# Optimization experiments

Hardware: AMD Instinct MI355X
Metric: run time of the kernel (lower is better)

## Reference

```python
import jax, jax.numpy as jnp
import numpy as np

KS = 2            # kernel_size
NUM_SHARED = 3    # len(num_shared_channels)
NBR_PARAM = 3     # nbr_param_layers
COUT = 128        # num_shared_channels[-1] == num_inputs
NUM_INPUTS = 128
D_R = 320         # ts2vec_output_dims
GEN_LEN = NBR_PARAM * COUT * COUT * KS


def _causal_conv(x, w, b, d):
    # x: [N, Ci, T], w: [Co, Ci, K], b: [Co]; left-pad (K-1)*d == pad+chomp in torch
    N, Ci, T = x.shape
    K = w.shape[-1]
    pad = (K - 1) * d
    xp = jnp.pad(x, ((0, 0), (0, 0), (pad, 0)))
    out = jnp.zeros((N, w.shape[0], T), dtype=x.dtype)
    for k in range(K):  # K==2, tiny static loop
        out = out + jnp.einsum('oc,nct->not', w[:, :, k], xp[:, :, k * d:k * d + T])
    return out + b[None, :, None]


def _causal_conv_group(x, w, d):
    # groups=N conv with per-sample weights. x: [N, C, T], w: [N, Co, C, K], no bias
    N, C, T = x.shape
    K = w.shape[-1]
    pad = (K - 1) * d
    xp = jnp.pad(x, ((0, 0), (0, 0), (pad, 0)))
    out = jnp.zeros((N, w.shape[1], T), dtype=x.dtype)
    for k in range(K):
        out = out + jnp.einsum('noc,nct->not', w[..., k], xp[:, :, k * d:k * d + T])
    return out


def setup_inputs() -> dict:
    key = jax.random.key(0)
    ks = jax.random.split(key, 12)
    N, T = 16, 1024
    x = jax.random.normal(ks[0], (N, T, NUM_INPUTS), dtype=jnp.float32)
    r = jax.random.normal(ks[1], (N, D_R), dtype=jnp.float32)
    # shared TemporalBlock params (in==out==COUT, so no downsample conv)
    wscale = 1.0 / np.sqrt(COUT * KS)
    shared_w1 = wscale * jax.random.normal(ks[2], (NUM_SHARED, COUT, COUT, KS), dtype=jnp.float32)
    shared_b1 = 0.01 * jax.random.normal(ks[3], (NUM_SHARED, COUT), dtype=jnp.float32)
    shared_w2 = wscale * jax.random.normal(ks[4], (NUM_SHARED, COUT, COUT, KS), dtype=jnp.float32)
    shared_b2 = 0.01 * jax.random.normal(ks[5], (NUM_SHARED, COUT), dtype=jnp.float32)
    # hypernetwork (f_param_generator) + additive base weights (last_conv_layers)
    fparam_W = 0.01 * jax.random.normal(ks[6], (GEN_LEN, D_R), dtype=jnp.float32)
    fparam_b = 0.01 * jax.random.normal(ks[7], (GEN_LEN,), dtype=jnp.float32)
    last_bias = 0.001 * jax.random.normal(ks[8], (GEN_LEN,), dtype=jnp.float32) + 1.0 / (KS * COUT)
    # output head
    lin_W = (1.0 / np.sqrt(COUT)) * jax.random.normal(ks[9], (NUM_INPUTS, COUT), dtype=jnp.float32)
    lin_b = 0.01 * jax.random.normal(ks[10], (NUM_INPUTS,), dtype=jnp.float32)
    return {"x": x, "r": r, "f_out_same_in_size": 1,
            "shared_w1": shared_w1, "shared_b1": shared_b1,
            "shared_w2": shared_w2, "shared_b2": shared_b2,
            "fparam_W": fparam_W, "fparam_b": fparam_b, "last_bias": last_bias,
            "lin_W": lin_W, "lin_b": lin_b}


def reference(x, r, f_out_same_in_size, shared_w1, shared_b1, shared_w2, shared_b2,
              fparam_W, fparam_b, last_bias, lin_W, lin_b):
    N, T, _ = x.shape
    h = jnp.swapaxes(x, 1, 2)  # [N, C, T]
    # shared TemporalBlocks (dropout p=0 -> identity)
    for i in range(NUM_SHARED):
        d = 2 ** i
        res = h
        a = jax.nn.relu(_causal_conv(h, shared_w1[i], shared_b1[i], d))
        a = jax.nn.relu(_causal_conv(a, shared_w2[i], shared_b2[i], d))
        h = jax.nn.relu(a + res)
    # hypernet-generated per-sample grouped conv layers
    gen = r @ fparam_W.T + fparam_b + last_bias           # [N, GEN_LEN]
    allw = gen.reshape(NBR_PARAM, N, COUT, COUT, KS)      # same layout as torch .view
    for i in range(NBR_PARAM):
        d = 2 ** (NUM_SHARED + i)
        res = h
        c = _causal_conv_group(h, allw[i], d)
        h = jax.nn.relu(jax.nn.relu(c) + res)             # relu(dropout(relu(c)) + res), p=0
    out = jnp.einsum('nct,oc->nto', h, lin_W) + lin_b     # [N, T, NUM_INPUTS]
    if not f_out_same_in_size:
        out = out[:, -1, :]
    return out
```

## Files before the change

kernel.cpp:

```cpp
#include <hip/hip_runtime.h>

#define NB    16
#define TLEN  1024
#define CCH   128
#define DR    320

typedef _Float16 h8 __attribute__((ext_vector_type(8)));
typedef _Float16 h4 __attribute__((ext_vector_type(4)));
typedef _Float16 h2 __attribute__((ext_vector_type(2)));
typedef float    f4 __attribute__((ext_vector_type(4)));

__device__ __forceinline__ void gload16h(const _Float16* g, _Float16* l) {
  __builtin_amdgcn_global_load_lds(
      (const __attribute__((address_space(1))) void*)g,
      (__attribute__((address_space(3))) void*)l, 16, 0, 0);
}
__device__ __forceinline__ void gload16f(const float* g, float* l) {
  __builtin_amdgcn_global_load_lds(
      (const __attribute__((address_space(1))) void*)g,
      (__attribute__((address_space(3))) void*)l, 16, 0, 0);
}

__global__ __launch_bounds__(256) void k_init(const float* __restrict__ x,
                                              const float* __restrict__ w1,
                                              const float* __restrict__ w2,
                                              const float* __restrict__ linw,
                                              const float* __restrict__ fb,
                                              const float* __restrict__ lb,
                                              _Float16* __restrict__ h0,
                                              _Float16* __restrict__ Wsh,
                                              _Float16* __restrict__ linWh,
                                              float* __restrict__ fblb2) {
  int i = blockIdx.x * 256 + threadIdx.x;
  const float4* src = (const float4*)x + (size_t)i * 2;
  float4 a = src[0], b = src[1];
  h8 v;
  v[0] = (_Float16)a.x; v[1] = (_Float16)a.y; v[2] = (_Float16)a.z; v[3] = (_Float16)a.w;
  v[4] = (_Float16)b.x; v[5] = (_Float16)b.y; v[6] = (_Float16)b.z; v[7] = (_Float16)b.w;
  *(h8*)(h0 + (size_t)i * 8) = v;

  if (i < 6 * 32768) {
    int c = i & 127, k = (i >> 7) & 1, o = (i >> 8) & 127, i3 = i >> 15;
    const float* srcw = (i3 < 3) ? (w1 + i3 * 32768) : (w2 + (i3 - 3) * 32768);
    Wsh[i] = (_Float16)srcw[(o * 128 + c) * 2 + k];
  }
  if (i < 16384) linWh[i] = (_Float16)linw[i];
  if (i < 98304) fblb2[i] = fb[i] + lb[i];
}

struct SGen {
  float buf[3][32 * DR];
  float csc[4][16][16];
  float fbl[512];
};
struct SPair {
  _Float16 hin[84 * 128];
  _Float16 a[80 * 128];
};
union alignas(16) SU { SGen g; SPair p; };

__device__ __forceinline__ void gen_body(SGen& S, int bid, int tid,
                                         const float* __restrict__ r,
                                         const float* __restrict__ fW,
                                         const float* __restrict__ fblb2,
                                         _Float16* __restrict__ wg) {
  constexpr int NT = 16;
  const size_t rbase = (size_t)bid * 512;

  const int l = tid & 63, w = tid >> 6;
  const int l15 = l & 15, lh = l >> 4;
  const int rt = w >> 1, kh = w & 1;

  f4 rx[5], ry[5];
  const float* rp = r + l15 * DR + kh * 160 + lh * 8;
#pragma unroll
  for (int cb = 0; cb < 5; cb++) {
    rx[cb] = *(const f4*)(rp + cb * 32);
    ry[cb] = *(const f4*)(rp + cb * 32 + 4);
  }
  if (tid < 128) gload16f(fblb2 + rbase + tid * 4, S.fbl + tid * 4);
#pragma unroll
  for (int t = 0; t < 3; t++) {
    const float* s = fW + (rbase + (size_t)t * 32) * DR;
#pragma unroll
    for (int i = 0; i < 10; i++) {
      int f = tid + i * 256;
      gload16f(s + (size_t)f * 4, (float*)S.buf[t] + (size_t)f * 4);
    }
  }
  h8 bfr[5];
#pragma unroll
  for (int cb = 0; cb < 5; cb++) {
    h8 v;
    v[0] = (_Float16)rx[cb][0]; v[1] = (_Float16)rx[cb][1];
    v[2] = (_Float16)rx[cb][2]; v[3] = (_Float16)rx[cb][3];
    v[4] = (_Float16)ry[cb][0]; v[5] = (_Float16)ry[cb][1];
    v[6] = (_Float16)ry[cb][2]; v[7] = (_Float16)ry[cb][3];
    bfr[cb] = v;
  }
  asm volatile("s_waitcnt vmcnt(20) lgkmcnt(0)" ::: "memory");
  __builtin_amdgcn_s_barrier();
  __builtin_amdgcn_sched_barrier(0);

  const int rn = tid >> 4, rk = (tid >> 3) & 1, rcq = tid & 7;

  for (int j = 0; j < NT; j++) {
    const float* bp = (const float*)S.buf[j % 3];
    f4 acc = {0.f, 0.f, 0.f, 0.f};
    const float* arow = bp + (rt * 16 + l15) * DR + kh * 160 + lh * 8;
#pragma unroll
    for (int cb = 0; cb < 5; cb++) {
      f4 x = *(const f4*)(arow + cb * 32);
      f4 y = *(const f4*)(arow + cb * 32 + 4);
      h8 a;
      a[0] = (_Float16)x[0]; a[1] = (_Float16)x[1];
      a[2] = (_Float16)x[2]; a[3] = (_Float16)x[3];
      a[4] = (_Float16)y[0]; a[5] = (_Float16)y[1];
      a[6] = (_Float16)y[2]; a[7] = (_Float16)y[3];
      acc = __builtin_amdgcn_mfma_f32_16x16x32_f16(a, bfr[cb], acc, 0, 0, 0);
    }
#pragma unroll
    for (int rr = 0; rr < 4; rr++) S.csc[w][lh * 4 + rr][l15] = acc[rr];

    asm volatile("s_waitcnt lgkmcnt(0)" ::: "memory");
    __builtin_amdgcn_s_barrier();
    __builtin_amdgcn_sched_barrier(0);

    {
      const unsigned g32 = (unsigned)(rbase + (size_t)j * 32);
      const unsigned G = g32 >> 15, o = (g32 >> 8) & 127u, c0 = (g32 & 255u) >> 1;
      h2 v2;
#pragma unroll
      for (int i = 0; i < 2; i++) {
        int rl32 = (rcq * 2 + i) * 2 + rk;
        int hp = (rl32 >> 4) * 2, rr2 = rl32 & 15;
        float s = S.csc[hp][rr2][rn] + S.csc[hp + 1][rr2][rn] + S.fbl[j * 32 + rl32];
        v2[i] = (_Float16)s;
      }
      unsigned q = 3u * (unsigned)rn + G;
      *(h2*)&wg[(((size_t)q * 128 + o) * 2 + rk) * 128 + c0 + rcq * 2] = v2;
    }
    __builtin_amdgcn_sched_barrier(0);

    if (j + 3 < NT) {
      float* dstb = (float*)S.buf[j % 3];
      const float* src = fW + (rbase + (size_t)(j + 3) * 32) * DR;
#pragma unroll
      for (int i = 0; i < 10; i++) {
        int f = tid + i * 256;
        gload16f(src + (size_t)f * 4, dstb + (size_t)f * 4);
      }
    }

    if (j + 4 <= NT)
      asm volatile("s_waitcnt vmcnt(20) lgkmcnt(0)" ::: "memory");
    else if (j + 3 == NT)
      asm volatile("s_waitcnt vmcnt(10) lgkmcnt(0)" ::: "memory");
    else
      asm volatile("s_waitcnt vmcnt(0) lgkmcnt(0)" ::: "memory");
    __builtin_amdgcn_s_barrier();
    __builtin_amdgcn_sched_barrier(0);
  }
}

template <int D>
__device__ __forceinline__ void pair_body(SPair& S, int tx, int n, int tid,
                                          const _Float16* in, _Float16* out,
                                          const _Float16* w1p, const _Float16* w2p,
                                          const float* b1p, const float* b2p) {
  constexpr int HA = 16;
  constexpr int HI = HA + D;
  constexpr int RIN = 80 + D;
  static_assert(RIN * 128 <= sizeof(SPair::hin) / sizeof(_Float16), "hin size");
  _Float16* hin_l = S.hin;
  _Float16* a_l = S.a;
  const int t0 = tx * 64;
  const _Float16* inN = in + (size_t)n * (TLEN * CCH);

  if (tx == 0) {
    for (int f = tid; f < HI * 16; f += 256)
      *(int4*)(hin_l + (size_t)f * 8) = make_int4(0, 0, 0, 0);
    for (int f = HI * 16 + tid; f < RIN * 16; f += 256) {
      int p = f >> 4, l16 = f & 15;
      int c8 = (l16 ^ (p & 15)) << 3;
      gload16h(inN + (t0 - HI + p) * 128 + c8, hin_l + f * 8);
    }
  } else {
    for (int f = tid; f < RIN * 16; f += 256) {
      int p = f >> 4, l16 = f & 15;
      int c8 = (l16 ^ (p & 15)) << 3;
      gload16h(inN + (t0 - HI + p) * 128 + c8, hin_l + f * 8);
    }
  }
  __syncthreads();

  const int l = tid & 63, w = tid >> 6;
  const int l15 = l & 15, lh = l >> 4;
  const int o0 = w * 32;

  f4 acc1[2][5] = {};
#pragma unroll
  for (int tap = 0; tap < 2; tap++) {
#pragma unroll
    for (int cb = 0; cb < 4; cb++) {
      const int c0 = cb * 32 + lh * 8;
      h8 a[2], bfr[5];
#pragma unroll
      for (int i2 = 0; i2 < 2; i2++) {
        int o = o0 + i2 * 16 + l15;
        a[i2] = *(const h8*)&w1p[(o * 2 + tap) * 128 + c0];
      }
#pragma unroll
      for (int jt = 0; jt < 5; jt++) {
        int p = jt * 16 + l15 + tap * D;
        int cs = c0 ^ ((p & 15) << 3);
        bfr[jt] = *(const h8*)&hin_l[p * 128 + cs];
      }
#pragma unroll
      for (int i2 = 0; i2 < 2; i2++)
#pragma unroll
        for (int jt = 0; jt < 5; jt++)
          acc1[i2][jt] = __builtin_amdgcn_mfma_f32_16x16x32_f16(
              a[i2], bfr[jt], acc1[i2][jt], 0, 0, 0);
    }
  }
#pragma unroll
  for (int i2 = 0; i2 < 2; i2++) {
    f4 bv = *(const f4*)&b1p[o0 + i2 * 16 + lh * 4];
    const int base8 = o0 + i2 * 16 + (lh >> 1) * 8;
    const int sub = (lh & 1) * 4;
#pragma unroll
    for (int jt = 0; jt < 5; jt++) {
      int p = jt * 16 + l15;
      h4 sv;
      if (tx == 0 && jt == 0) {
        sv[0] = sv[1] = sv[2] = sv[3] = (_Float16)0.f;
      } else {
        f4 v = acc1[i2][jt];
#pragma unroll
        for (int rr = 0; rr < 4; rr++) sv[rr] = (_Float16)fmaxf(v[rr] + bv[rr], 0.f);
      }
      *(h4*)&a_l[p * 128 + (base8 ^ ((p & 15) << 3)) + sub] = sv;
    }
  }
  __syncthreads();

  f4 acc2[2][4] = {};
#pragma unroll
  for (int tap = 0; tap < 2; tap++) {
#pragma unroll
    for (int cb = 0; cb < 4; cb++) {
      const int c0 = cb * 32 + lh * 8;
      h8 a[2], bfr[4];
#pragma unroll
      for (int i2 = 0; i2 < 2; i2++) {
        int o = o0 + i2 * 16 + l15;
        a[i2] = *(const h8*)&w2p[(o * 2 + tap) * 128 + c0];
      }
#pragma unroll
      for (int jt = 0; jt < 4; jt++) {
        int pa = jt * 16 + l15 + (HA - D) + tap * D;
        int cs = c0 ^ ((pa & 15) << 3);
        bfr[jt] = *(const h8*)&a_l[pa * 128 + cs];
      }
#pragma unroll
      for (int i2 = 0; i2 < 2; i2++)
#pragma unroll
        for (int jt = 0; jt < 4; jt++)
          acc2[i2][jt] = __builtin_amdgcn_mfma_f32_16x16x32_f16(
              a[i2], bfr[jt], acc2[i2][jt], 0, 0, 0);
    }
  }

  _Float16* outN = out + (size_t)n * (TLEN * CCH);
#pragma unroll
  for (int i2 = 0; i2 < 2; i2++) {
    f4 bv = *(const f4*)&b2p[o0 + i2 * 16 + lh * 4];
    const int base8 = o0 + i2 * 16 + (lh >> 1) * 8;
    const int sub = (lh & 1) * 4;
#pragma unroll
    for (int jt = 0; jt < 4; jt++) {
      int t = t0 + jt * 16 + l15;
      int pr = jt * 16 + l15 + HA + D;
      h4 rv = *(const h4*)&hin_l[pr * 128 + (base8 ^ ((pr & 15) << 3)) + sub];
      f4 v = acc2[i2][jt];
      h4 sv;
#pragma unroll
      for (int rr = 0; rr < 4; rr++) {
        float z = fmaxf(v[rr] + bv[rr], 0.f);
        sv[rr] = (_Float16)fmaxf(z + (float)rv[rr], 0.f);
      }
      *(h4*)&outN[t * 128 + o0 + i2 * 16 + lh * 4] = sv;
    }
  }
}

__global__ __launch_bounds__(256, 1) void k_genpair(
    const float* __restrict__ r, const float* __restrict__ fW,
    const float* __restrict__ fblb2, _Float16* __restrict__ wg,
    const _Float16* __restrict__ h0, _Float16* __restrict__ h1,
    const _Float16* __restrict__ Wsh,
    const float* __restrict__ b1, const float* __restrict__ b2) {
  __shared__ SU su;
  const int bid = blockIdx.x, tid = threadIdx.x;
  if (bid < 192) {
    gen_body(su.g, bid, tid, r, fW, fblb2, wg);
  } else {
    int q = bid - 192;
    pair_body<1>(su.p, q & 15, q >> 4, tid, h0, h1,
                 Wsh, Wsh + 3 * 32768, b1, b2);
  }
}

template <int D>
__global__ __launch_bounds__(256) void k_pair(const _Float16* __restrict__ in,
                                              _Float16* __restrict__ out,
                                              const _Float16* __restrict__ w1p,
                                              const _Float16* __restrict__ w2p,
                                              const float* __restrict__ b1p,
                                              const float* __restrict__ b2p) {
  __shared__ SPair sp;
  pair_body<D>(sp, blockIdx.x, blockIdx.y, threadIdx.x, in, out, w1p, w2p,
               b1p, b2p);
}

template <int D>
__global__ __launch_bounds__(256) void k_gconv(const _Float16* __restrict__ in,
                                               _Float16* __restrict__ out,
                                               const _Float16* __restrict__ wBase) {
  __shared__ _Float16 Wl[256 * 128];
  __shared__ _Float16 hl[(64 + D) * 128];
  const int tid = threadIdx.x;
  const int n = blockIdx.y, t0 = blockIdx.x * 64;
  const _Float16* inN = in + (size_t)n * (TLEN * CCH);
  const _Float16* wp = wBase + (size_t)n * 32768;

  for (int f = tid; f < 4096; f += 256) {
    int row = f >> 4, l16 = f & 15;
    int c8 = (l16 ^ ((row >> 1) & 15)) << 3;
    gload16h(wp + row * 128 + c8, Wl + f * 8);
  }
  if (blockIdx.x == 0) {
    for (int f = tid; f < D * 16; f += 256)
      *(int4*)(hl + (size_t)f * 8) = make_int4(0, 0, 0, 0);
    for (int f = D * 16 + tid; f < (64 + D) * 16; f += 256) {
      int p = f >> 4, l16 = f & 15;
      int c8 = (l16 ^ (p & 15)) << 3;
      gload16h(inN + (t0 - D + p) * 128 + c8, hl + f * 8);
    }
  } else {
    for (int f = tid; f < (64 + D) * 16; f += 256) {
      int p = f >> 4, l16 = f & 15;
      int c8 = (l16 ^ (p & 15)) << 3;
      gload16h(inN + (t0 - D + p) * 128 + c8, hl + f * 8);
    }
  }
  __syncthreads();

  const int l = tid & 63, w = tid >> 6;
  const int l15 = l & 15, lh = l >> 4;
  const int o0 = w * 32;
  f4 acc[2][4] = {};

#pragma unroll
  for (int tap = 0; tap < 2; tap++) {
#pragma unroll
    for (int cb = 0; cb < 4; cb++) {
      const int c0 = cb * 32 + 8 * lh;
      h8 a[2], bfr[4];
#pragma unroll
      for (int i2 = 0; i2 < 2; i2++) {
        int o = o0 + i2 * 16 + l15;
        int cs = c0 ^ ((o & 15) << 3);
        a[i2] = *(const h8*)&Wl[(o * 2 + tap) * 128 + cs];
      }
#pragma unroll
      for (int jt = 0; jt < 4; jt++) {
        int p = jt * 16 + l15 + tap * D;
        int cs = c0 ^ ((p & 15) << 3);
        bfr[jt] = *(const h8*)&hl[p * 128 + cs];
      }
#pragma unroll
      for (int i2 = 0; i2 < 2; i2++)
#pragma unroll
        for (int jt = 0; jt < 4; jt++)
          acc[i2][jt] = __builtin_amdgcn_mfma_f32_16x16x32_f16(
              a[i2], bfr[jt], acc[i2][jt], 0, 0, 0);
    }
  }

  _Float16* outN = out + (size_t)n * (TLEN * CCH);
#pragma unroll
  for (int i2 = 0; i2 < 2; i2++) {
    const int base8 = o0 + i2 * 16 + (lh >> 1) * 8;
    const int sub = (lh & 1) * 4;
#pragma unroll
    for (int jt = 0; jt < 4; jt++) {
      int t = t0 + jt * 16 + l15;
      int pr = jt * 16 + l15 + D;
      h4 rv = *(const h4*)&hl[pr * 128 + (base8 ^ ((pr & 15) << 3)) + sub];
      f4 v = acc[i2][jt];
      h4 sv;
#pragma unroll
      for (int rr = 0; rr < 4; rr++) {
        float z = fmaxf(v[rr], 0.f);
        sv[rr] = (_Float16)fmaxf(z + (float)rv[rr], 0.f);
      }
      *(h4*)&outN[t * 128 + o0 + i2 * 16 + lh * 4] = sv;
    }
  }
}

__global__ __launch_bounds__(256) void k_glin(const _Float16* __restrict__ in,
                                              float* __restrict__ outp,
                                              const _Float16* __restrict__ wBase,
                                              const _Float16* __restrict__ linWh,
                                              const float* __restrict__ lbias) {
  constexpr int D = 32;
  __shared__ _Float16 Wl[256 * 128];
  __shared__ _Float16 hl[(64 + D) * 128];
  __shared__ _Float16 a_l[64 * 128];
  const int tid = threadIdx.x;
  const int n = blockIdx.y, t0 = blockIdx.x * 64;
  const _Float16* inN = in + (size_t)n * (TLEN * CCH);
  const _Float16* wp = wBase + (size_t)n * 32768;

  for (int f = tid; f < 4096; f += 256) {
    int row = f >> 4, l16 = f & 15;
    int c8 = (l16 ^ ((row >> 1) & 15)) << 3;
    gload16h(wp + row * 128 + c8, Wl + f * 8);
  }
  if (blockIdx.x == 0) {
    for (int f = tid; f < D * 16; f += 256)
      *(int4*)(hl + (size_t)f * 8) = make_int4(0, 0, 0, 0);
    for (int f = D * 16 + tid; f < (64 + D) * 16; f += 256) {
      int p = f >> 4, l16 = f & 15;
      int c8 = (l16 ^ (p & 15)) << 3;
      gload16h(inN + (t0 - D + p) * 128 + c8, hl + f * 8);
    }
  } else {
    for (int f = tid; f < (64 + D) * 16; f += 256) {
      int p = f >> 4, l16 = f & 15;
      int c8 = (l16 ^ (p & 15)) << 3;
      gload16h(inN + (t0 - D + p) * 128 + c8, hl + f * 8);
    }
  }
  __syncthreads();

  const int l = tid & 63, w = tid >> 6;
  const int l15 = l & 15, lh = l >> 4;
  const int o0 = w * 32;
  f4 acc[2][4] = {};

#pragma unroll
  for (int tap = 0; tap < 2; tap++) {
#pragma unroll
    for (int cb = 0; cb < 4; cb++) {
      const int c0 = cb * 32 + 8 * lh;
      h8 a[2], bfr[4];
#pragma unroll
      for (int i2 = 0; i2 < 2; i2++) {
        int o = o0 + i2 * 16 + l15;
        int cs = c0 ^ ((o & 15) << 3);
        a[i2] = *(const h8*)&Wl[(o * 2 + tap) * 128 + cs];
      }
#pragma unroll
      for (int jt = 0; jt < 4; jt++) {
        int p = jt * 16 + l15 + tap * D;
        int cs = c0 ^ ((p & 15) << 3);
        bfr[jt] = *(const h8*)&hl[p * 128 + cs];
      }
#pragma unroll
      for (int i2 = 0; i2 < 2; i2++)
#pragma unroll
        for (int jt = 0; jt < 4; jt++)
          acc[i2][jt] = __builtin_amdgcn_mfma_f32_16x16x32_f16(
              a[i2], bfr[jt], acc[i2][jt], 0, 0, 0);
    }
  }

#pragma unroll
  for (int i2 = 0; i2 < 2; i2++) {
    const int base8 = o0 + i2 * 16 + (lh >> 1) * 8;
    const int sub = (lh & 1) * 4;
#pragma unroll
    for (int jt = 0; jt < 4; jt++) {
      int p = jt * 16 + l15;
      int pr = p + D;
      h4 rv = *(const h4*)&hl[pr * 128 + (base8 ^ ((pr & 15) << 3)) + sub];
      f4 v = acc[i2][jt];
      h4 sv;
#pragma unroll
      for (int rr = 0; rr < 4; rr++) {
        float z = fmaxf(v[rr], 0.f);
        sv[rr] = (_Float16)fmaxf(z + (float)rv[rr], 0.f);
      }
      *(h4*)&a_l[p * 128 + (base8 ^ (l15 << 3)) + sub] = sv;
    }
  }
  __syncthreads();

  f4 acc3[2][4] = {};
#pragma unroll
  for (int cb = 0; cb < 4; cb++) {
    const int c0 = cb * 32 + lh * 8;
    h8 a[2], bfr[4];
#pragma unroll
    for (int i2 = 0; i2 < 2; i2++) {
      int o = o0 + i2 * 16 + l15;
      a[i2] = *(const h8*)&linWh[o * 128 + c0];
    }
#pragma unroll
    for (int jt = 0; jt < 4; jt++) {
      int p = jt * 16 + l15;
      int cs = c0 ^ ((p & 15) << 3);
      bfr[jt] = *(const h8*)&a_l[p * 128 + cs];
    }
#pragma unroll
    for (int i2 = 0; i2 < 2; i2++)
#pragma unroll
      for (int jt = 0; jt < 4; jt++)
        acc3[i2][jt] = __builtin_amdgcn_mfma_f32_16x16x32_f16(
            a[i2], bfr[jt], acc3[i2][jt], 0, 0, 0);
  }

#pragma unroll
  for (int i2 = 0; i2 < 2; i2++) {
    int o = o0 + i2 * 16 + lh * 4;
    f4 bv = *(const f4*)&lbias[o];
#pragma unroll
    for (int jt = 0; jt < 4; jt++) {
      int t = t0 + jt * 16 + l15;
      f4 v = acc3[i2][jt];
      float4 sv = make_float4(v[0] + bv[0], v[1] + bv[1], v[2] + bv[2], v[3] + bv[3]);
      *(float4*)&outp[((size_t)n * TLEN + t) * CCH + o] = sv;
    }
  }
}

extern "C" void kernel_launch(void* const* d_in, const int* in_sizes, int n_in,
                              void* d_out, int out_size, void* d_ws, size_t ws_size,
                              hipStream_t stream) {
  const float* x  = (const float*)d_in[0];
  const float* r  = (const float*)d_in[1];
  const float* w1 = (const float*)d_in[3];
  const float* b1 = (const float*)d_in[4];
  const float* w2 = (const float*)d_in[5];
  const float* b2 = (const float*)d_in[6];
  const float* fW = (const float*)d_in[7];
  const float* fb = (const float*)d_in[8];
  const float* lb = (const float*)d_in[9];
  const float* lw = (const float*)d_in[10];
  const float* lbias = (const float*)d_in[11];
  float* out = (float*)d_out;

  _Float16* h0    = (_Float16*)d_ws;
  _Float16* h1    = h0 + 2097152;
  _Float16* Wsh   = h1 + 2097152;
  _Float16* linWh = Wsh + 393216;
  _Float16* Wg    = linWh + 16384;
  float*    fblb2 = (float*)(Wg + 1572864);

  k_init<<<1024, 256, 0, stream>>>(x, w1, w2, lw, fb, lb, h0, Wsh, linWh, fblb2);
  k_genpair<<<448, 256, 0, stream>>>(r, fW, fblb2, Wg, h0, h1, Wsh, b1, b2);

  const dim3 cg(16, 16);
  k_pair<2><<<cg, 256, 0, stream>>>(h1, h0, Wsh + 1 * 32768, Wsh + 4 * 32768,
                                    b1 + 128, b2 + 128);
  k_pair<4><<<cg, 256, 0, stream>>>(h0, h1, Wsh + 2 * 32768, Wsh + 5 * 32768,
                                    b1 + 256, b2 + 256);
  k_gconv<8> <<<cg, 256, 0, stream>>>(h1, h0, Wg);
  k_gconv<16><<<cg, 256, 0, stream>>>(h0, h1, Wg + 524288);
  k_glin<<<cg, 256, 0, stream>>>(h1, out, Wg + 1048576, linWh, lbias);
}
```

Measured before the change: 78.04 us.

## Fuse three grouped conv layers and output linear into one halo-recompute kernel

Replaces the two k_gconv launches and k_glin with a single k_group kernel. Each block loads a 56-row causal halo plus its 64-step tile once, then runs the three dilated grouped convs back to back in shared memory, swapping weights between stages, before the output linear. This removes two launches and the global round trips of intermediate activations. In exchange the halo rows are recomputed redundantly in every block, the weight reloads sit between stages, and occupancy is limited by the large LDS footprint.

Result: faster. 75.34 us (-3.5%).

```diff
diff --git a/kernel.cpp b/kernel.cpp
--- a/kernel.cpp
+++ b/kernel.cpp
@@ -324,50 +324,22 @@
                b1p, b2p);
 }
 
-template <int D>
-__global__ __launch_bounds__(256) void k_gconv(const _Float16* __restrict__ in,
-                                               _Float16* __restrict__ out,
-                                               const _Float16* __restrict__ wBase) {
-  __shared__ _Float16 Wl[256 * 128];
-  __shared__ _Float16 hl[(64 + D) * 128];
-  const int tid = threadIdx.x;
-  const int n = blockIdx.y, t0 = blockIdx.x * 64;
-  const _Float16* inN = in + (size_t)n * (TLEN * CCH);
-  const _Float16* wp = wBase + (size_t)n * 32768;
-
-  for (int f = tid; f < 4096; f += 256) {
-    int row = f >> 4, l16 = f & 15;
-    int c8 = (l16 ^ ((row >> 1) & 15)) << 3;
-    gload16h(wp + row * 128 + c8, Wl + f * 8);
-  }
-  if (blockIdx.x == 0) {
-    for (int f = tid; f < D * 16; f += 256)
-      *(int4*)(hl + (size_t)f * 8) = make_int4(0, 0, 0, 0);
-    for (int f = D * 16 + tid; f < (64 + D) * 16; f += 256) {
-      int p = f >> 4, l16 = f & 15;
-      int c8 = (l16 ^ (p & 15)) << 3;
-      gload16h(inN + (t0 - D + p) * 128 + c8, hl + f * 8);
-    }
-  } else {
-    for (int f = tid; f < (64 + D) * 16; f += 256) {
-      int p = f >> 4, l16 = f & 15;
-      int c8 = (l16 ^ (p & 15)) << 3;
-      gload16h(inN + (t0 - D + p) * 128 + c8, hl + f * 8);
-    }
-  }
-  __syncthreads();
-
+template <int D, int NJ>
+__device__ __forceinline__ void gstage(const _Float16* __restrict__ Wl,
+                                       const _Float16* __restrict__ inb,
+                                       _Float16* __restrict__ outb,
+                                       int zlim, int tid) {
   const int l = tid & 63, w = tid >> 6;
   const int l15 = l & 15, lh = l >> 4;
   const int o0 = w * 32;
-  f4 acc[2][4] = {};
+  f4 acc[2][NJ] = {};
 
 #pragma unroll
   for (int tap = 0; tap < 2; tap++) {
 #pragma unroll
     for (int cb = 0; cb < 4; cb++) {
       const int c0 = cb * 32 + 8 * lh;
-      h8 a[2], bfr[4];
+      h8 a[2], bfr[NJ];
 #pragma unroll
       for (int i2 = 0; i2 < 2; i2++) {
         int o = o0 + i2 * 16 + l15;
@@ -375,131 +347,107 @@
         a[i2] = *(const h8*)&Wl[(o * 2 + tap) * 128 + cs];
       }
 #pragma unroll
-      for (int jt = 0; jt < 4; jt++) {
+      for (int jt = 0; jt < NJ; jt++) {
         int p = jt * 16 + l15 + tap * D;
         int cs = c0 ^ ((p & 15) << 3);
-        bfr[jt] = *(const h8*)&hl[p * 128 + cs];
+        bfr[jt] = *(const h8*)&inb[p * 128 + cs];
       }
 #pragma unroll
       for (int i2 = 0; i2 < 2; i2++)
 #pragma unroll
-        for (int jt = 0; jt < 4; jt++)
+        for (int jt = 0; jt < NJ; jt++)
           acc[i2][jt] = __builtin_amdgcn_mfma_f32_16x16x32_f16(
               a[i2], bfr[jt], acc[i2][jt], 0, 0, 0);
     }
   }
 
-  _Float16* outN = out + (size_t)n * (TLEN * CCH);
 #pragma unroll
   for (int i2 = 0; i2 < 2; i2++) {
     const int base8 = o0 + i2 * 16 + (lh >> 1) * 8;
     const int sub = (lh & 1) * 4;
 #pragma unroll
-    for (int jt = 0; jt < 4; jt++) {
-      int t = t0 + jt * 16 + l15;
-      int pr = jt * 16 + l15 + D;
-      h4 rv = *(const h4*)&hl[pr * 128 + (base8 ^ ((pr & 15) << 3)) + sub];
-      f4 v = acc[i2][jt];
+    for (int jt = 0; jt < NJ; jt++) {
+      int rrow = jt * 16 + l15;
+      int pr = rrow + D;
       h4 sv;
-#pragma unroll
-      for (int rr = 0; rr < 4; rr++) {
-        float z = fmaxf(v[rr], 0.f);
-        sv[rr] = (_Float16)fmaxf(z + (float)rv[rr], 0.f);
-      }
-      *(h4*)&outN[t * 128 + o0 + i2 * 16 + lh * 4] = sv;
-    }
-  }
-}
-
-__global__ __launch_bounds__(256) void k_glin(const _Float16* __restrict__ in,
-                                              float* __restrict__ outp,
-                                              const _Float16* __restrict__ wBase,
-                                              const _Float16* __restrict__ linWh,
-                                              const float* __restrict__ lbias) {
-  constexpr int D = 32;
+      if (rrow < zlim) {
+        sv[0] = sv[1] = sv[2] = sv[3] = (_Float16)0.f;
+      } else {
+        h4 rv = *(const h4*)&inb[pr * 128 + (base8 ^ ((pr & 15) << 3)) + sub];
+        f4 v = acc[i2][jt];
+#pragma unroll
+        for (int rr = 0; rr < 4; rr++) {
+          float z = fmaxf(v[rr], 0.f);
+          sv[rr] = (_Float16)fmaxf(z + (float)rv[rr], 0.f);
+        }
+      }
+      *(h4*)&outb[rrow * 128 + (base8 ^ (l15 << 3)) + sub] = sv;
+    }
+  }
+}
+
+__global__ __launch_bounds__(256, 1) void k_group(const _Float16* __restrict__ in,
+                                                  float* __restrict__ outp,
+                                                  const _Float16* __restrict__ wg,
+                                                  const _Float16* __restrict__ linWh,
+                                                  const float* __restrict__ lbias) {
+  __shared__ _Float16 bufA[120 * 128];
+  __shared__ _Float16 bufB[112 * 128];
   __shared__ _Float16 Wl[256 * 128];
-  __shared__ _Float16 hl[(64 + D) * 128];
-  __shared__ _Float16 a_l[64 * 128];
   const int tid = threadIdx.x;
-  const int n = blockIdx.y, t0 = blockIdx.x * 64;
+  const int tx = blockIdx.x, n = blockIdx.y;
+  const int t0 = tx * 64;
   const _Float16* inN = in + (size_t)n * (TLEN * CCH);
-  const _Float16* wp = wBase + (size_t)n * 32768;
-
+  const _Float16* wp1 = wg + (size_t)n * 32768;
+  const _Float16* wp2 = wg + 524288 + (size_t)n * 32768;
+  const _Float16* wp3 = wg + 1048576 + (size_t)n * 32768;
+
+  if (tx == 0) {
+    for (int f = tid; f < 56 * 16; f += 256)
+      *(int4*)(bufA + (size_t)f * 8) = make_int4(0, 0, 0, 0);
+    for (int f = 56 * 16 + tid; f < 120 * 16; f += 256) {
+      int p = f >> 4, l16 = f & 15;
+      int c8 = (l16 ^ (p & 15)) << 3;
+      gload16h(inN + (t0 - 56 + p) * 128 + c8, bufA + f * 8);
+    }
+  } else {
+    for (int f = tid; f < 120 * 16; f += 256) {
+      int p = f >> 4, l16 = f & 15;
+      int c8 = (l16 ^ (p & 15)) << 3;
+      gload16h(inN + (t0 - 56 + p) * 128 + c8, bufA + f * 8);
+    }
+  }
   for (int f = tid; f < 4096; f += 256) {
     int row = f >> 4, l16 = f & 15;
     int c8 = (l16 ^ ((row >> 1) & 15)) << 3;
-    gload16h(wp + row * 128 + c8, Wl + f * 8);
-  }
-  if (blockIdx.x == 0) {
-    for (int f = tid; f < D * 16; f += 256)
-      *(int4*)(hl + (size_t)f * 8) = make_int4(0, 0, 0, 0);
-    for (int f = D * 16 + tid; f < (64 + D) * 16; f += 256) {
-      int p = f >> 4, l16 = f & 15;
-      int c8 = (l16 ^ (p & 15)) << 3;
-      gload16h(inN + (t0 - D + p) * 128 + c8, hl + f * 8);
-    }
-  } else {
-    for (int f = tid; f < (64 + D) * 16; f += 256) {
-      int p = f >> 4, l16 = f & 15;
-      int c8 = (l16 ^ (p & 15)) << 3;
-      gload16h(inN + (t0 - D + p) * 128 + c8, hl + f * 8);
-    }
-  }
+    gload16h(wp1 + row * 128 + c8, Wl + f * 8);
+  }
+  __syncthreads();
+
+  gstage<8, 7>(Wl, bufA, bufB, (tx == 0) ? 48 : 0, tid);
+  __syncthreads();
+  for (int f = tid; f < 4096; f += 256) {
+    int row = f >> 4, l16 = f & 15;
+    int c8 = (l16 ^ ((row >> 1) & 15)) << 3;
+    gload16h(wp2 + row * 128 + c8, Wl + f * 8);
+  }
+  __syncthreads();
+
+  gstage<16, 6>(Wl, bufB, bufA, (tx == 0) ? 32 : 0, tid);
+  __syncthreads();
+  for (int f = tid; f < 4096; f += 256) {
+    int row = f >> 4, l16 = f & 15;
+    int c8 = (l16 ^ ((row >> 1) & 15)) << 3;
+    gload16h(wp3 + row * 128 + c8, Wl + f * 8);
+  }
+  __syncthreads();
+
+  gstage<32, 4>(Wl, bufA, bufB, 0, tid);
   __syncthreads();
 
   const int l = tid & 63, w = tid >> 6;
   const int l15 = l & 15, lh = l >> 4;
   const int o0 = w * 32;
-  f4 acc[2][4] = {};
-
-#pragma unroll
-  for (int tap = 0; tap < 2; tap++) {
-#pragma unroll
-    for (int cb = 0; cb < 4; cb++) {
-      const int c0 = cb * 32 + 8 * lh;
-      h8 a[2], bfr[4];
-#pragma unroll
-      for (int i2 = 0; i2 < 2; i2++) {
-        int o = o0 + i2 * 16 + l15;
-        int cs = c0 ^ ((o & 15) << 3);
-        a[i2] = *(const h8*)&Wl[(o * 2 + tap) * 128 + cs];
-      }
-#pragma unroll
-      for (int jt = 0; jt < 4; jt++) {
-        int p = jt * 16 + l15 + tap * D;
-        int cs = c0 ^ ((p & 15) << 3);
-        bfr[jt] = *(const h8*)&hl[p * 128 + cs];
-      }
-#pragma unroll
-      for (int i2 = 0; i2 < 2; i2++)
-#pragma unroll
-        for (int jt = 0; jt < 4; jt++)
-          acc[i2][jt] = __builtin_amdgcn_mfma_f32_16x16x32_f16(
-              a[i2], bfr[jt], acc[i2][jt], 0, 0, 0);
-    }
-  }
-
-#pragma unroll
-  for (int i2 = 0; i2 < 2; i2++) {
-    const int base8 = o0 + i2 * 16 + (lh >> 1) * 8;
-    const int sub = (lh & 1) * 4;
-#pragma unroll
-    for (int jt = 0; jt < 4; jt++) {
-      int p = jt * 16 + l15;
-      int pr = p + D;
-      h4 rv = *(const h4*)&hl[pr * 128 + (base8 ^ ((pr & 15) << 3)) + sub];
-      f4 v = acc[i2][jt];
-      h4 sv;
-#pragma unroll
-      for (int rr = 0; rr < 4; rr++) {
-        float z = fmaxf(v[rr], 0.f);
-        sv[rr] = (_Float16)fmaxf(z + (float)rv[rr], 0.f);
-      }
-      *(h4*)&a_l[p * 128 + (base8 ^ (l15 << 3)) + sub] = sv;
-    }
-  }
-  __syncthreads();
-
   f4 acc3[2][4] = {};
 #pragma unroll
   for (int cb = 0; cb < 4; cb++) {
@@ -514,7 +462,7 @@
     for (int jt = 0; jt < 4; jt++) {
       int p = jt * 16 + l15;
       int cs = c0 ^ ((p & 15) << 3);
-      bfr[jt] = *(const h8*)&a_l[p * 128 + cs];
+      bfr[jt] = *(const h8*)&bufB[p * 128 + cs];
     }
 #pragma unroll
     for (int i2 = 0; i2 < 2; i2++)
@@ -569,7 +517,5 @@
                                     b1 + 128, b2 + 128);
   k_pair<4><<<cg, 256, 0, stream>>>(h0, h1, Wsh + 2 * 32768, Wsh + 5 * 32768,
                                     b1 + 256, b2 + 256);
-  k_gconv<8> <<<cg, 256, 0, stream>>>(h1, h0, Wg);
-  k_gconv<16><<<cg, 256, 0, stream>>>(h0, h1, Wg + 524288);
-  k_glin<<<cg, 256, 0, stream>>>(h1, out, Wg + 1048576, linWh, lbias);
-}
+  k_group<<<cg, 256, 0, stream>>>(h1, out, Wg, linWh, lbias);
+}
```
